# Kernel tuning notes

Measured on AMD Instinct MI355X. Metric: run time of the kernel, lower is better.

## Reference

```python
import jax, jax.numpy as jnp
import numpy as np

N, E, T, HID, LH = 16000, 256000, 5, 64, 128


def setup_inputs():
    key = jax.random.key(0)
    ks = jax.random.split(key, 16)
    rn = lambda k, s, sc=0.05: jax.random.normal(k, s, jnp.float32) * sc
    return {
        "x": jax.random.normal(ks[0], (N, T), jnp.float32),
        "edge_index": jax.random.randint(ks[1], (2, E), 0, N),
        "gcn_w": rn(ks[2], (HID, 1)),
        "gcn_b": rn(ks[3], (HID,)),
        "w_ih0": rn(ks[4], (4 * LH, HID)),
        "w_hh0": rn(ks[5], (4 * LH, LH)),
        "b_ih0": rn(ks[6], (4 * LH,)),
        "b_hh0": rn(ks[7], (4 * LH,)),
        "w_ih1": rn(ks[8], (4 * LH, LH)),
        "w_hh1": rn(ks[9], (4 * LH, LH)),
        "b_ih1": rn(ks[10], (4 * LH,)),
        "b_hh1": rn(ks[11], (4 * LH,)),
        "pw1": rn(ks[12], (LH // 2, LH)),
        "pb1": rn(ks[13], (LH // 2,)),
        "pw2": rn(ks[14], (1, LH // 2)),
        "pb2": rn(ks[15], (1,)),
    }


def _gcn(x, src, dst, n, W, b):
    # PyG GCNConv: linear, add self-loops, symmetric D^-1/2 (A+I) D^-1/2, scatter-sum at dst, bias
    loop = jnp.arange(n, dtype=src.dtype)
    s = jnp.concatenate([src, loop])
    d = jnp.concatenate([dst, loop])
    deg = jnp.zeros((n,), x.dtype).at[d].add(jnp.ones((), x.dtype))
    dinv = jnp.where(deg > 0, jax.lax.rsqrt(deg), jnp.zeros((), x.dtype))
    norm = (dinv[s] * dinv[d])[:, None]
    h = x @ W.T  # [n, HID]
    return jax.ops.segment_sum(h[s] * norm, d, num_segments=n) + b


def _lstm_layer(xs, Wih, Whh, bih, bhh):
    # torch.nn.LSTM single layer, gate order (i, f, g, o), zero initial state
    H = Whh.shape[1]
    def step(carry, xt):
        h, c = carry
        g = xt @ Wih.T + bih + h @ Whh.T + bhh
        i, f, gg, o = jnp.split(g, 4, axis=-1)
        c = jax.nn.sigmoid(f) * c + jax.nn.sigmoid(i) * jnp.tanh(gg)
        h = jax.nn.sigmoid(o) * jnp.tanh(c)
        return (h, c), h
    h0 = jnp.zeros((xs.shape[1], H), xs.dtype)
    _, ys = jax.lax.scan(step, (h0, h0), xs)
    return ys


def reference(x, edge_index, gcn_w, gcn_b, w_ih0, w_hh0, b_ih0, b_hh0,
              w_ih1, w_hh1, b_ih1, b_hh1, pw1, pb1, pw2, pb2):
    n, t = x.shape
    x_t = x[:, -1:]
    xb = x.T.reshape(-1, 1)  # [T*N, 1]
    offs = (jnp.arange(t, dtype=edge_index.dtype) * n)[:, None, None]
    # flat row-major reshape of [T,2,E] -> [2,T*E], exactly as in the torch source
    eb = jnp.reshape(edge_index[None, :, :] + offs, (2, -1))
    h = jax.nn.relu(_gcn(xb, eb[0], eb[1], t * n, gcn_w, gcn_b))
    seq = h.reshape(t, n, -1)  # [T, N, HID]
    y0 = _lstm_layer(seq, w_ih0, w_hh0, b_ih0, b_hh0)
    y1 = _lstm_layer(y0, w_ih1, w_hh1, b_ih1, b_hh1)  # inter-layer dropout = eval mode (identity)
    last = y1[-1]  # [N, LH]
    delta = jax.nn.relu(last @ pw1.T + pb1) @ pw2.T + pb2  # predictor MLP, dropout off
    return x_t + delta
```

## Files before the change

kernel.cpp:

```cpp
#include <hip/hip_runtime.h>
#include <hip/hip_bf16.h>

#define Nn 16000
#define Ee 256000
#define Tt 5
#define GATES 512
#define NREP 8

typedef _Float16 f16;
typedef __attribute__((ext_vector_type(8))) _Float16 f16x8;
typedef __attribute__((ext_vector_type(4))) float f32x4;

#define OFF_DINV 0
#define OFF_AGGR  (OFF_DINV + Nn)
#define OFF_DEGR  (OFF_AGGR + NREP*Nn*Tt)
#define OFF_B0    (OFF_DEGR + NREP*Nn)
#define OFF_B1    (OFF_B0 + GATES)
#define OFF_W0S   (OFF_B1 + GATES)
#define OFF_W1S   (OFF_W0S + 512*192/2)
#define OFF_PWS   (OFF_W1S + 512*256/2)
#define OFF_END   (OFF_PWS + 64*128/2)

__device__ __forceinline__ float fsig(float x) { return 1.f / (1.f + __expf(-x)); }
__device__ __forceinline__ float ftanh(float x) { return 1.f - 2.f / (1.f + __expf(2.f * x)); }

__device__ __forceinline__ unsigned xcc_id() {
    unsigned x;
    asm volatile("s_getreg_b32 %0, hwreg(HW_REG_XCC_ID)" : "=s"(x));
    return x & (NREP - 1);
}

__global__ void prep_weights(const float* __restrict__ w_ih0, const float* __restrict__ w_hh0,
                             const float* __restrict__ b_ih0, const float* __restrict__ b_hh0,
                             const float* __restrict__ w_ih1, const float* __restrict__ w_hh1,
                             const float* __restrict__ b_ih1, const float* __restrict__ b_hh1,
                             const float* __restrict__ pw1,
                             f16* __restrict__ W0S, f16* __restrict__ W1S, f16* __restrict__ pwS,
                             float* __restrict__ B0, float* __restrict__ B1,
                             int* __restrict__ degr, float* __restrict__ aggr) {
    int b = blockIdx.x, t = threadIdx.x;
    if (b < 512) {
        if (t < 192) {
            int q = b, k = t;
            float v = (k < 64) ? w_ih0[q * 64 + k] : w_hh0[q * 128 + (k - 64)];
            int g = (q & 127) >> 4, l = q & 15, gate = q >> 7;
            int kt = k >> 5, quad = (k >> 3) & 3, j = k & 7;
            W0S[(((g * 6 + kt) * 4 + gate) * 64 + quad * 16 + l) * 8 + j] = (f16)v;
        }
    } else if (b < 1024) {
        int q = b - 512, k = t;
        float v = (k < 128) ? w_ih1[q * 128 + k] : w_hh1[q * 128 + (k - 128)];
        int g = (q & 127) >> 4, l = q & 15, gate = q >> 7;
        int kt = k >> 5, quad = (k >> 3) & 3, j = k & 7;
        W1S[(((g * 8 + kt) * 4 + gate) * 64 + quad * 16 + l) * 8 + j] = (f16)v;
    } else if (b < 1028) {
        int idx = (b - 1024) * 256 + t;
        if (idx < 512) B0[idx] = b_ih0[idx] + b_hh0[idx];
        else           B1[idx - 512] = b_ih1[idx - 512] + b_hh1[idx - 512];
    } else if (b < 1092) {
        if (t < 128) {
            int u = b - 1028, k = t;
            int g = u >> 4, lp = u & 15;
            int kt = k >> 5, quad = (k >> 3) & 3, j = k & 7;
            pwS[((g * 4 + kt) * 64 + quad * 16 + lp) * 8 + j] = (f16)pw1[u * 128 + k];
        }
    } else if (b < 1592) {
        int n = (b - 1092) * 256 + t;
        if (n < NREP * Nn) degr[n] = 0;
    } else {
        int n = (b - 1592) * 256 + t;
        if (n < NREP * Nn * Tt) aggr[n] = 0.f;
    }
}

__global__ void deg_count(const int* __restrict__ ei, int* __restrict__ degr) {
    int e = blockIdx.x * blockDim.x + threadIdx.x;
    if (e >= Ee) return;
    int* p = &degr[xcc_id() * Nn + ei[Ee + e]];
    __hip_atomic_fetch_add(p, 1, __ATOMIC_RELAXED, __HIP_MEMORY_SCOPE_WORKGROUP);
}

__global__ void dinv_kernel(const int* __restrict__ degr, float* __restrict__ dinv) {
    int n = blockIdx.x * blockDim.x + threadIdx.x;
    if (n >= Nn) return;
    int deg = 1;
    #pragma unroll
    for (int r = 0; r < NREP; ++r) deg += degr[r * Nn + n];
    dinv[n] = rsqrtf((float)deg);
}

__global__ void edge_scatter(const float* __restrict__ x, const int* __restrict__ ei,
                             const float* __restrict__ dinv, float* __restrict__ aggr) {
    int idx = blockIdx.x * blockDim.x + threadIdx.x;
    if (idx >= Ee * Tt) return;
    int e = idx / Tt, t = idx - e * Tt;
    int s = ei[e], d = ei[Ee + e];
    float v = x[s * Tt + t] * dinv[s];
    float* p = aggr + (size_t)xcc_id() * (Nn * Tt) + (size_t)d * Tt + t;
    __hip_atomic_fetch_add(p, v, __ATOMIC_RELAXED, __HIP_MEMORY_SCOPE_WORKGROUP);
}

__global__ __launch_bounds__(512, 2) void recur_all(
    const float* __restrict__ aggr, const float* __restrict__ dinv,
    const float* __restrict__ gw, const float* __restrict__ gb,
    const f16* __restrict__ W0S, const f16* __restrict__ W1S,
    const float* __restrict__ B0, const float* __restrict__ B1,
    const f16* __restrict__ pwS, const float* __restrict__ pb1,
    const float* __restrict__ pw2, const float* __restrict__ pb2,
    const float* __restrict__ x, float* __restrict__ out) {
    __shared__ f16 h0buf[2][32 * 128];
    __shared__ f16 h1buf[2][32 * 128];
    __shared__ float sAgg[32 * Tt];
    const int tid = threadIdx.x;
    const int lane = tid & 63;
    const int uq = tid >> 6;
    const int l = lane & 15;
    const int quad = lane >> 4;
    const int n0 = blockIdx.x * 32;
    const int u = uq * 16 + l;
    const int uch = u >> 3;
    const int ulo = u & 7;

    if (tid < 32 * Tt) {
        int nl = tid / Tt, t = tid - nl * Tt;
        int n = n0 + nl;
        size_t off = (size_t)n * Tt + t;
        float s = 0.f;
        #pragma unroll
        for (int r = 0; r < NREP; ++r) s += aggr[(size_t)r * (Nn * Tt) + off];
        float dv = dinv[n];
        sAgg[nl * Tt + t] = s * dv + x[off] * dv * dv;
    }

    const float bI0 = B0[u], bF0 = B0[128 + u], bG0 = B0[256 + u], bO0 = B0[384 + u];
    const float bI1 = B1[u], bF1 = B1[128 + u], bG1 = B1[256 + u], bO1 = B1[384 + u];

    f32x4 c0s[2], c1s[2];
    #pragma unroll
    for (int i = 0; i < 2; ++i) {
        c0s[i] = (f32x4){0.f, 0.f, 0.f, 0.f};
        c1s[i] = (f32x4){0.f, 0.f, 0.f, 0.f};
    }
    __syncthreads();

    f32x4 acc[2][4];
    #pragma unroll 1
    for (int t = 0; t < Tt; ++t) {
        const int cur = t & 1;
        const f16* h0r = h0buf[cur];
        const f16* h1r = h1buf[cur];
        f16* h0w = h0buf[cur ^ 1];
        f16* h1w = h1buf[cur ^ 1];

        #pragma unroll
        for (int i = 0; i < 2; ++i)
            #pragma unroll
            for (int g = 0; g < 4; ++g) acc[i][g] = (f32x4){0.f, 0.f, 0.f, 0.f};
        float an[2];
        #pragma unroll
        for (int i = 0; i < 2; ++i)
            an[i] = sAgg[(i * 16 + l) * Tt + t];

        #pragma unroll
        for (int kt = 0; kt < 2; ++kt) {
            f16x8 af[2];
            #pragma unroll
            for (int j = 0; j < 8; ++j) {
                int k = kt * 32 + quad * 8 + j;
                float gwj = gw[k], gbj = gb[k];
                #pragma unroll
                for (int i = 0; i < 2; ++i)
                    af[i][j] = (f16)fmaxf(gwj * an[i] + gbj, 0.f);
            }
            const f16* bp = W0S + ((size_t)(uq * 6 + kt) * 4) * 512 + lane * 8;
            #pragma unroll
            for (int g = 0; g < 4; ++g) {
                f16x8 b = *(const f16x8*)(bp + g * 512);
                #pragma unroll
                for (int i = 0; i < 2; ++i)
                    acc[i][g] = __builtin_amdgcn_mfma_f32_16x16x32_f16(af[i], b, acc[i][g], 0, 0, 0);
            }
        }
        if (t > 0) {
            #pragma unroll 2
            for (int kt = 2; kt < 6; ++kt) {
                int ub = (kt - 2) * 4 + quad;
                f16x8 af[2];
                #pragma unroll
                for (int i = 0; i < 2; ++i)
                    af[i] = *(const f16x8*)&h0r[(i * 16 + l) * 128 + ((ub ^ l) << 3)];
                const f16* bp = W0S + ((size_t)(uq * 6 + kt) * 4) * 512 + lane * 8;
                #pragma unroll
                for (int g = 0; g < 4; ++g) {
                    f16x8 b = *(const f16x8*)(bp + g * 512);
                    #pragma unroll
                    for (int i = 0; i < 2; ++i)
                        acc[i][g] = __builtin_amdgcn_mfma_f32_16x16x32_f16(af[i], b, acc[i][g], 0, 0, 0);
                }
            }
        }
        #pragma unroll
        for (int i = 0; i < 2; ++i) {
            f32x4 cc = c0s[i];
            #pragma unroll
            for (int r = 0; r < 4; ++r) {
                float i_ = fsig(acc[i][0][r] + bI0);
                float f_ = fsig(acc[i][1][r] + bF0);
                float g_ = ftanh(acc[i][2][r] + bG0);
                float o_ = fsig(acc[i][3][r] + bO0);
                float cn = f_ * cc[r] + i_ * g_;
                cc[r] = cn;
                float hn = o_ * ftanh(cn);
                int node = i * 16 + quad * 4 + r;
                h0w[node * 128 + (((uch ^ (node & 15)) << 3) | ulo)] = (f16)hn;
            }
            c0s[i] = cc;
        }
        __syncthreads();

        #pragma unroll
        for (int i = 0; i < 2; ++i)
            #pragma unroll
            for (int g = 0; g < 4; ++g) acc[i][g] = (f32x4){0.f, 0.f, 0.f, 0.f};

        {
            int ktmax = (t == 0) ? 4 : 8;
            #pragma unroll 2
            for (int kt = 0; kt < ktmax; ++kt) {
                const f16* hb = (kt < 4) ? h0w : h1r;
                int ub = (kt & 3) * 4 + quad;
                f16x8 af[2];
                #pragma unroll
                for (int i = 0; i < 2; ++i)
                    af[i] = *(const f16x8*)&hb[(i * 16 + l) * 128 + ((ub ^ l) << 3)];
                const f16* bp = W1S + ((size_t)(uq * 8 + kt) * 4) * 512 + lane * 8;
                #pragma unroll
                for (int g = 0; g < 4; ++g) {
                    f16x8 b = *(const f16x8*)(bp + g * 512);
                    #pragma unroll
                    for (int i = 0; i < 2; ++i)
                        acc[i][g] = __builtin_amdgcn_mfma_f32_16x16x32_f16(af[i], b, acc[i][g], 0, 0, 0);
                }
            }
        }
        #pragma unroll
        for (int i = 0; i < 2; ++i) {
            f32x4 cc = c1s[i];
            #pragma unroll
            for (int r = 0; r < 4; ++r) {
                float i_ = fsig(acc[i][0][r] + bI1);
                float f_ = fsig(acc[i][1][r] + bF1);
                float g_ = ftanh(acc[i][2][r] + bG1);
                float o_ = fsig(acc[i][3][r] + bO1);
                float cn = f_ * cc[r] + i_ * g_;
                cc[r] = cn;
                float hn = o_ * ftanh(cn);
                int node = i * 16 + quad * 4 + r;
                h1w[node * 128 + (((uch ^ (node & 15)) << 3) | ulo)] = (f16)hn;
            }
            c1s[i] = cc;
        }
        __syncthreads();
    }

    const f16* h1f = h1buf[1];
    if (uq < 2) {
        f32x4 hacc[4];
        #pragma unroll
        for (int g = 0; g < 4; ++g) hacc[g] = (f32x4){0.f, 0.f, 0.f, 0.f};
        #pragma unroll
        for (int kt = 0; kt < 4; ++kt) {
            int ub = kt * 4 + quad;
            f16x8 a = *(const f16x8*)&h1f[(uq * 16 + l) * 128 + ((ub ^ l) << 3)];
            #pragma unroll
            for (int g = 0; g < 4; ++g) {
                f16x8 b = *(const f16x8*)(pwS + (size_t)(g * 4 + kt) * 512 + lane * 8);
                hacc[g] = __builtin_amdgcn_mfma_f32_16x16x32_f16(a, b, hacc[g], 0, 0, 0);
            }
        }
        float yr[4] = {0.f, 0.f, 0.f, 0.f};
        #pragma unroll
        for (int g = 0; g < 4; ++g) {
            float pb = pb1[g * 16 + l];
            float pw = pw2[g * 16 + l];
            #pragma unroll
            for (int r = 0; r < 4; ++r)
                yr[r] += fmaxf(hacc[g][r] + pb, 0.f) * pw;
        }
        #pragma unroll
        for (int m = 1; m <= 8; m <<= 1) {
            #pragma unroll
            for (int r = 0; r < 4; ++r) yr[r] += __shfl_xor(yr[r], m);
        }
        if (l < 4) {
            float v = (l == 0) ? yr[0] : (l == 1) ? yr[1] : (l == 2) ? yr[2] : yr[3];
            int node = n0 + uq * 16 + quad * 4 + l;
            out[node] = x[node * Tt + (Tt - 1)] + v + pb2[0];
        }
    }
}

extern "C" void kernel_launch(void* const* d_in, const int* in_sizes, int n_in,
                              void* d_out, int out_size, void* d_ws, size_t ws_size,
                              hipStream_t stream) {
    const float* x      = (const float*)d_in[0];
    const int*   ei     = (const int*)d_in[1];
    const float* gcn_w  = (const float*)d_in[2];
    const float* gcn_b  = (const float*)d_in[3];
    const float* w_ih0  = (const float*)d_in[4];
    const float* w_hh0  = (const float*)d_in[5];
    const float* b_ih0  = (const float*)d_in[6];
    const float* b_hh0  = (const float*)d_in[7];
    const float* w_ih1  = (const float*)d_in[8];
    const float* w_hh1  = (const float*)d_in[9];
    const float* b_ih1  = (const float*)d_in[10];
    const float* b_hh1  = (const float*)d_in[11];
    const float* pw1    = (const float*)d_in[12];
    const float* pb1    = (const float*)d_in[13];
    const float* pw2    = (const float*)d_in[14];
    const float* pb2    = (const float*)d_in[15];
    float* out = (float*)d_out;

    float* wsf  = (float*)d_ws;
    float* dinv = wsf + OFF_DINV;
    float* aggr = wsf + OFF_AGGR;
    int*   degr = (int*)(wsf + OFF_DEGR);
    float* B0   = wsf + OFF_B0;
    float* B1   = wsf + OFF_B1;
    f16*   W0S  = (f16*)(wsf + OFF_W0S);
    f16*   W1S  = (f16*)(wsf + OFF_W1S);
    f16*   pwS  = (f16*)(wsf + OFF_PWS);

    prep_weights<<<4092, 256, 0, stream>>>(w_ih0, w_hh0, b_ih0, b_hh0,
                                           w_ih1, w_hh1, b_ih1, b_hh1, pw1,
                                           W0S, W1S, pwS, B0, B1, degr, aggr);
    deg_count<<<(Ee + 255) / 256, 256, 0, stream>>>(ei, degr);
    dinv_kernel<<<(Nn + 255) / 256, 256, 0, stream>>>(degr, dinv);
    edge_scatter<<<(Ee * Tt + 255) / 256, 256, 0, stream>>>(x, ei, dinv, aggr);

    recur_all<<<Nn / 32, 512, 0, stream>>>(aggr, dinv, gcn_w, gcn_b, W0S, W1S, B0, B1,
                                           pwS, pb1, pw2, pb2, x, out);
}
```

Baseline: 203.9 us.

## Skew LSTM layers so layer-1 step t and layer-0 step t+1 share one barrier

The two-layer LSTM recurrence is software-pipelined. Layer 0 step 0 is peeled off, and each loop iteration then computes layer 1 at step t together with layer 0 at step t+1, reusing the same h0 A-fragments for both weight sets. This cuts the block barriers per timestep from two to one and shares LDS reads of h0. The cell states move from registers to 32 KB of LDS, which adds LDS traffic and may lower occupancy under the 512x2 launch bounds.

After: 221.5 us. 8.6% more time.

```diff
diff --git a/kernel.cpp b/kernel.cpp
--- a/kernel.cpp
+++ b/kernel.cpp
@@ -110,6 +110,8 @@
     const float* __restrict__ x, float* __restrict__ out) {
     __shared__ f16 h0buf[2][32 * 128];
     __shared__ f16 h1buf[2][32 * 128];
+    __shared__ float c0buf[32 * 128];
+    __shared__ float c1buf[32 * 128];
     __shared__ float sAgg[32 * Tt];
     const int tid = threadIdx.x;
     const int lane = tid & 63;
@@ -134,33 +136,17 @@
 
     const float bI0 = B0[u], bF0 = B0[128 + u], bG0 = B0[256 + u], bO0 = B0[384 + u];
     const float bI1 = B1[u], bF1 = B1[128 + u], bG1 = B1[256 + u], bO1 = B1[384 + u];
-
-    f32x4 c0s[2], c1s[2];
-    #pragma unroll
-    for (int i = 0; i < 2; ++i) {
-        c0s[i] = (f32x4){0.f, 0.f, 0.f, 0.f};
-        c1s[i] = (f32x4){0.f, 0.f, 0.f, 0.f};
-    }
     __syncthreads();
 
-    f32x4 acc[2][4];
-    #pragma unroll 1
-    for (int t = 0; t < Tt; ++t) {
-        const int cur = t & 1;
-        const f16* h0r = h0buf[cur];
-        const f16* h1r = h1buf[cur];
-        f16* h0w = h0buf[cur ^ 1];
-        f16* h1w = h1buf[cur ^ 1];
-
+    {
+        f32x4 acc0[2][4];
         #pragma unroll
         for (int i = 0; i < 2; ++i)
             #pragma unroll
-            for (int g = 0; g < 4; ++g) acc[i][g] = (f32x4){0.f, 0.f, 0.f, 0.f};
+            for (int g = 0; g < 4; ++g) acc0[i][g] = (f32x4){0.f, 0.f, 0.f, 0.f};
         float an[2];
         #pragma unroll
-        for (int i = 0; i < 2; ++i)
-            an[i] = sAgg[(i * 16 + l) * Tt + t];
-
+        for (int i = 0; i < 2; ++i) an[i] = sAgg[(i * 16 + l) * Tt + 0];
         #pragma unroll
         for (int kt = 0; kt < 2; ++kt) {
             f16x8 af[2];
@@ -178,87 +164,147 @@
                 f16x8 b = *(const f16x8*)(bp + g * 512);
                 #pragma unroll
                 for (int i = 0; i < 2; ++i)
-                    acc[i][g] = __builtin_amdgcn_mfma_f32_16x16x32_f16(af[i], b, acc[i][g], 0, 0, 0);
+                    acc0[i][g] = __builtin_amdgcn_mfma_f32_16x16x32_f16(af[i], b, acc0[i][g], 0, 0, 0);
+            }
+        }
+        #pragma unroll
+        for (int i = 0; i < 2; ++i) {
+            #pragma unroll
+            for (int r = 0; r < 4; ++r) {
+                int node = i * 16 + quad * 4 + r;
+                float i_ = fsig(acc0[i][0][r] + bI0);
+                float f_ = fsig(acc0[i][1][r] + bF0);  (void)f_;
+                float g_ = ftanh(acc0[i][2][r] + bG0);
+                float o_ = fsig(acc0[i][3][r] + bO0);
+                float cn = i_ * g_;
+                c0buf[node * 128 + u] = cn;
+                float hn = o_ * ftanh(cn);
+                h0buf[1][node * 128 + (((uch ^ (node & 15)) << 3) | ulo)] = (f16)hn;
+            }
+        }
+    }
+    __syncthreads();
+
+    #pragma unroll 1
+    for (int t = 0; t < Tt; ++t) {
+        const f16* h0r = h0buf[1 - (t & 1)];
+        const f16* h1r = h1buf[t & 1];
+        f16* h1w = h1buf[1 - (t & 1)];
+        f16* h0w = h0buf[t & 1];
+        const bool last = (t == Tt - 1);
+
+        f32x4 acc1[2][4], acc0[2][4];
+        #pragma unroll
+        for (int i = 0; i < 2; ++i)
+            #pragma unroll
+            for (int g = 0; g < 4; ++g) {
+                acc1[i][g] = (f32x4){0.f, 0.f, 0.f, 0.f};
+                acc0[i][g] = (f32x4){0.f, 0.f, 0.f, 0.f};
+            }
+
+        #pragma unroll 1
+        for (int kt = 0; kt < 4; ++kt) {
+            int ub = kt * 4 + quad;
+            f16x8 af[2];
+            #pragma unroll
+            for (int i = 0; i < 2; ++i)
+                af[i] = *(const f16x8*)&h0r[(i * 16 + l) * 128 + ((ub ^ l) << 3)];
+            const f16* bp1 = W1S + ((size_t)(uq * 8 + kt) * 4) * 512 + lane * 8;
+            #pragma unroll
+            for (int g = 0; g < 4; ++g) {
+                f16x8 b = *(const f16x8*)(bp1 + g * 512);
+                #pragma unroll
+                for (int i = 0; i < 2; ++i)
+                    acc1[i][g] = __builtin_amdgcn_mfma_f32_16x16x32_f16(af[i], b, acc1[i][g], 0, 0, 0);
+            }
+            if (!last) {
+                const f16* bp0 = W0S + ((size_t)(uq * 6 + kt + 2) * 4) * 512 + lane * 8;
+                #pragma unroll
+                for (int g = 0; g < 4; ++g) {
+                    f16x8 b = *(const f16x8*)(bp0 + g * 512);
+                    #pragma unroll
+                    for (int i = 0; i < 2; ++i)
+                        acc0[i][g] = __builtin_amdgcn_mfma_f32_16x16x32_f16(af[i], b, acc0[i][g], 0, 0, 0);
+                }
             }
         }
         if (t > 0) {
-            #pragma unroll 2
-            for (int kt = 2; kt < 6; ++kt) {
-                int ub = (kt - 2) * 4 + quad;
+            #pragma unroll 1
+            for (int kt = 0; kt < 4; ++kt) {
+                int ub = kt * 4 + quad;
                 f16x8 af[2];
                 #pragma unroll
                 for (int i = 0; i < 2; ++i)
-                    af[i] = *(const f16x8*)&h0r[(i * 16 + l) * 128 + ((ub ^ l) << 3)];
+                    af[i] = *(const f16x8*)&h1r[(i * 16 + l) * 128 + ((ub ^ l) << 3)];
+                const f16* bp1 = W1S + ((size_t)(uq * 8 + 4 + kt) * 4) * 512 + lane * 8;
+                #pragma unroll
+                for (int g = 0; g < 4; ++g) {
+                    f16x8 b = *(const f16x8*)(bp1 + g * 512);
+                    #pragma unroll
+                    for (int i = 0; i < 2; ++i)
+                        acc1[i][g] = __builtin_amdgcn_mfma_f32_16x16x32_f16(af[i], b, acc1[i][g], 0, 0, 0);
+                }
+            }
+        }
+        if (!last) {
+            float an[2];
+            #pragma unroll
+            for (int i = 0; i < 2; ++i) an[i] = sAgg[(i * 16 + l) * Tt + t + 1];
+            #pragma unroll
+            for (int kt = 0; kt < 2; ++kt) {
+                f16x8 af[2];
+                #pragma unroll
+                for (int j = 0; j < 8; ++j) {
+                    int k = kt * 32 + quad * 8 + j;
+                    float gwj = gw[k], gbj = gb[k];
+                    #pragma unroll
+                    for (int i = 0; i < 2; ++i)
+                        af[i][j] = (f16)fmaxf(gwj * an[i] + gbj, 0.f);
+                }
                 const f16* bp = W0S + ((size_t)(uq * 6 + kt) * 4) * 512 + lane * 8;
                 #pragma unroll
                 for (int g = 0; g < 4; ++g) {
                     f16x8 b = *(const f16x8*)(bp + g * 512);
                     #pragma unroll
                     for (int i = 0; i < 2; ++i)
-                        acc[i][g] = __builtin_amdgcn_mfma_f32_16x16x32_f16(af[i], b, acc[i][g], 0, 0, 0);
-                }
-            }
-        }
+                        acc0[i][g] = __builtin_amdgcn_mfma_f32_16x16x32_f16(af[i], b, acc0[i][g], 0, 0, 0);
+                }
+            }
+        }
+
         #pragma unroll
         for (int i = 0; i < 2; ++i) {
-            f32x4 cc = c0s[i];
             #pragma unroll
             for (int r = 0; r < 4; ++r) {
-                float i_ = fsig(acc[i][0][r] + bI0);
-                float f_ = fsig(acc[i][1][r] + bF0);
-                float g_ = ftanh(acc[i][2][r] + bG0);
-                float o_ = fsig(acc[i][3][r] + bO0);
-                float cn = f_ * cc[r] + i_ * g_;
-                cc[r] = cn;
+                int node = i * 16 + quad * 4 + r;
+                float co = (t == 0) ? 0.f : c1buf[node * 128 + u];
+                float i_ = fsig(acc1[i][0][r] + bI1);
+                float f_ = fsig(acc1[i][1][r] + bF1);
+                float g_ = ftanh(acc1[i][2][r] + bG1);
+                float o_ = fsig(acc1[i][3][r] + bO1);
+                float cn = f_ * co + i_ * g_;
+                c1buf[node * 128 + u] = cn;
                 float hn = o_ * ftanh(cn);
-                int node = i * 16 + quad * 4 + r;
-                h0w[node * 128 + (((uch ^ (node & 15)) << 3) | ulo)] = (f16)hn;
-            }
-            c0s[i] = cc;
-        }
-        __syncthreads();
-
-        #pragma unroll
-        for (int i = 0; i < 2; ++i)
-            #pragma unroll
-            for (int g = 0; g < 4; ++g) acc[i][g] = (f32x4){0.f, 0.f, 0.f, 0.f};
-
-        {
-            int ktmax = (t == 0) ? 4 : 8;
-            #pragma unroll 2
-            for (int kt = 0; kt < ktmax; ++kt) {
-                const f16* hb = (kt < 4) ? h0w : h1r;
-                int ub = (kt & 3) * 4 + quad;
-                f16x8 af[2];
-                #pragma unroll
-                for (int i = 0; i < 2; ++i)
-                    af[i] = *(const f16x8*)&hb[(i * 16 + l) * 128 + ((ub ^ l) << 3)];
-                const f16* bp = W1S + ((size_t)(uq * 8 + kt) * 4) * 512 + lane * 8;
-                #pragma unroll
-                for (int g = 0; g < 4; ++g) {
-                    f16x8 b = *(const f16x8*)(bp + g * 512);
-                    #pragma unroll
-                    for (int i = 0; i < 2; ++i)
-                        acc[i][g] = __builtin_amdgcn_mfma_f32_16x16x32_f16(af[i], b, acc[i][g], 0, 0, 0);
-                }
-            }
-        }
-        #pragma unroll
-        for (int i = 0; i < 2; ++i) {
-            f32x4 cc = c1s[i];
-            #pragma unroll
-            for (int r = 0; r < 4; ++r) {
-                float i_ = fsig(acc[i][0][r] + bI1);
-                float f_ = fsig(acc[i][1][r] + bF1);
-                float g_ = ftanh(acc[i][2][r] + bG1);
-                float o_ = fsig(acc[i][3][r] + bO1);
-                float cn = f_ * cc[r] + i_ * g_;
-                cc[r] = cn;
-                float hn = o_ * ftanh(cn);
-                int node = i * 16 + quad * 4 + r;
                 h1w[node * 128 + (((uch ^ (node & 15)) << 3) | ulo)] = (f16)hn;
             }
-            c1s[i] = cc;
+        }
+        if (!last) {
+            #pragma unroll
+            for (int i = 0; i < 2; ++i) {
+                #pragma unroll
+                for (int r = 0; r < 4; ++r) {
+                    int node = i * 16 + quad * 4 + r;
+                    float co = c0buf[node * 128 + u];
+                    float i_ = fsig(acc0[i][0][r] + bI0);
+                    float f_ = fsig(acc0[i][1][r] + bF0);
+                    float g_ = ftanh(acc0[i][2][r] + bG0);
+                    float o_ = fsig(acc0[i][3][r] + bO0);
+                    float cn = f_ * co + i_ * g_;
+                    c0buf[node * 128 + u] = cn;
+                    float hn = o_ * ftanh(cn);
+                    h0w[node * 128 + (((uch ^ (node & 15)) << 3) | ulo)] = (f16)hn;
+                }
+            }
         }
         __syncthreads();
     }
```
